# Kernel optimization log

Hardware: AMD Instinct MI355X
Metric: run time of the kernel (lower is better)

The kernel has to match this reference:

```python
import jax, jax.numpy as jnp
import numpy as np

HIDDEN = 2048
N_EXPERTS = 64
TOP_K = 2
N_TOKENS = 16384


def setup_inputs() -> dict:
    key = jax.random.key(0)
    k1, k2 = jax.random.split(key)
    x = jax.random.normal(k1, (N_TOKENS, HIDDEN), dtype=jnp.float32)
    gate_w = jax.random.normal(k2, (N_EXPERTS, HIDDEN), dtype=jnp.float32) * (1.0 / np.sqrt(HIDDEN))
    gate_b = jnp.zeros((N_EXPERTS,), dtype=jnp.float32)
    return {"x": x, "gate_w": gate_w, "gate_b": gate_b}


def reference(x, gate_w, gate_b):
    # gate: [N, H] @ [H, E] + [E] -> [N, E]
    router_logits = jnp.einsum("nh,eh->ne", x, gate_w) + gate_b
    # softmax over experts in fp32 (matches F.softmax(..., dim=1, dtype=float32))
    router_probs = jax.nn.softmax(router_logits.astype(jnp.float32), axis=1)
    # top-k experts per token
    router_weights, selected_experts_indices = jax.lax.top_k(router_probs, TOP_K)  # [N, K]
    router_weights = router_weights / jnp.sum(router_weights, axis=-1, keepdims=True)
    router_weights = router_weights.astype(x.dtype)
    # one-hot [N, K, E] -> permute(2,1,0) -> [E, K, N]
    expert_mask = jax.nn.one_hot(selected_experts_indices, N_EXPERTS, dtype=jnp.int64 if jax.config.jax_enable_x64 else jnp.int32)
    expert_mask = jnp.transpose(expert_mask, (2, 1, 0))
    return (router_logits, router_weights, selected_experts_indices, expert_mask)
```

## Files before the change

### kernel.cpp

```cpp
#include <hip/hip_runtime.h>
#include <hip/hip_bf16.h>
#include <math.h>

#define HIDDEN 2048
#define NEXP   64
#define NTOK   16384
#define NTGF   512

typedef __attribute__((ext_vector_type(8))) _Float16 f16x8;
typedef __attribute__((ext_vector_type(4))) float   f32x4;

__device__ __forceinline__ void split2_f16(float4 f0, float4 f1, f16x8& h, f16x8& l) {
    float e[8] = {f0.x, f0.y, f0.z, f0.w, f1.x, f1.y, f1.z, f1.w};
    f16x8 hv, lv;
#pragma unroll
    for (int i = 0; i < 8; ++i) {
        _Float16 hh = (_Float16)e[i];
        float r = e[i] - (float)hh;
        hv[i] = hh;
        lv[i] = (_Float16)r;
    }
    h = hv; l = lv;
}

__global__ __launch_bounds__(256) void prep_kernel(
    const float* __restrict__ gw, uint4* __restrict__ wh, uint4* __restrict__ wl)
{
    const int gid = blockIdx.x * 256 + threadIdx.x;
    const int c   = gid >> 9;
    const int e   = (gid >> 3) & 63;
    const int kgp = gid & 7;
    const int kg  = kgp ^ (e & 7);
    const float* src = gw + (size_t)e * HIDDEN + c * 64 + kg * 8;
    float4 s0 = *(const float4*)src;
    float4 s1 = *(const float4*)(src + 4);
    f16x8 h, l;
    split2_f16(s0, s1, h, l);
    wh[gid] = __builtin_bit_cast(uint4, h);
    wl[gid] = __builtin_bit_cast(uint4, l);
}

#define STAGE(cg, bo)                                                                     \
    _Pragma("unroll")                                                                     \
    for (int rr = 0; rr < 2; ++rr) {                                                      \
        const int s = rr * 256 + tid;                                                     \
        __builtin_amdgcn_global_load_lds(                                                 \
            (const __attribute__((address_space(1))) void*)(wh + (size_t)(cg) * 512 + s), \
            (__attribute__((address_space(3))) void*)&Bs[(bo) + s], 16, 0, 0);            \
        __builtin_amdgcn_global_load_lds(                                                 \
            (const __attribute__((address_space(1))) void*)(wl + (size_t)(cg) * 512 + s), \
            (__attribute__((address_space(3))) void*)&Bs[(bo) + 512 + s], 16, 0, 0);      \
    }

__global__ __launch_bounds__(256, 4) void gemm_kernel(
    const float* __restrict__ x,
    const uint4* __restrict__ wh,
    const uint4* __restrict__ wl,
    float* __restrict__ part,
    int klen)
{
    __shared__ uint4 Bs[2 * 1024];

    const int tid = threadIdx.x;
    const int l   = tid & 63;
    const int wv  = tid >> 6;
    const int kg  = blockIdx.y;
    const int kbase = kg * klen;
    const int nch   = klen >> 6;
    const int cg0   = kbase >> 6;
    const int t0    = blockIdx.x * 64 + wv * 16;

    const float4* xp = (const float4*)(x + (size_t)(t0 + (l & 15)) * HIDDEN + kbase) + ((l >> 4) * 2);

    const int lb = ((l & 15) << 3) | ((l >> 4) ^ (l & 7));

    f32x4 acc1[4], acc2[4];
#pragma unroll
    for (int eg = 0; eg < 4; ++eg) {
        acc1[eg] = (f32x4){0.f, 0.f, 0.f, 0.f};
        acc2[eg] = (f32x4){0.f, 0.f, 0.f, 0.f};
    }

    STAGE(cg0, 0)
    float4 a0 = xp[0], a1 = xp[1], a2 = xp[8], a3 = xp[9];
    __syncthreads();

    for (int c = 0; c < nch; ++c) {
        const int buf = c & 1;
        float4 n0 = a0, n1 = a1, n2 = a2, n3 = a3;
        if (c + 1 < nch) {
            STAGE(cg0 + c + 1, (buf ^ 1) * 1024)
            const int fb = (c + 1) * 16;
            n0 = xp[fb + 0]; n1 = xp[fb + 1]; n2 = xp[fb + 8]; n3 = xp[fb + 9];
        }

#pragma unroll
        for (int ks = 0; ks < 2; ++ks) {
            f16x8 ah, al;
            split2_f16(ks ? a2 : a0, ks ? a3 : a1, ah, al);
            const int ib = buf * 1024 + (lb ^ (ks << 2));
#pragma unroll
            for (int eg = 0; eg < 4; ++eg) {
                f16x8 bh = __builtin_bit_cast(f16x8, Bs[ib + eg * 128]);
                f16x8 bl = __builtin_bit_cast(f16x8, Bs[ib + 512 + eg * 128]);
                acc1[eg] = __builtin_amdgcn_mfma_f32_16x16x32_f16(ah, bh, acc1[eg], 0, 0, 0);
                acc2[eg] = __builtin_amdgcn_mfma_f32_16x16x32_f16(ah, bl, acc2[eg], 0, 0, 0);
                acc2[eg] = __builtin_amdgcn_mfma_f32_16x16x32_f16(al, bh, acc2[eg], 0, 0, 0);
            }
        }
        a0 = n0; a1 = n1; a2 = n2; a3 = n3;
        __syncthreads();
    }

    float* pp = part + ((size_t)kg * NTOK + t0) * NEXP;
#pragma unroll
    for (int eg = 0; eg < 4; ++eg)
#pragma unroll
        for (int i = 0; i < 4; ++i)
            pp[(size_t)((l >> 4) * 4 + i) * NEXP + eg * 16 + (l & 15)] =
                acc1[eg][i] + acc2[eg][i];
}

__global__ __launch_bounds__(256) void finish_kernel(
    const float* __restrict__ part,
    const float* __restrict__ bias_g,
    float* __restrict__ logits,
    float* __restrict__ weights,
    float* __restrict__ idxf,
    float* __restrict__ mask,
    int KS)
{
    __shared__ float Ls[32][65];
    __shared__ int selA[32], selB[32];

    const int tid = threadIdx.x;
    const int bm0 = blockIdx.x * 32;
    const int tn  = tid & 15;
    const int tm  = tid >> 4;

    float4 acc[2];
#pragma unroll
    for (int i = 0; i < 2; ++i) acc[i] = make_float4(0.f, 0.f, 0.f, 0.f);

    for (int kg = 0; kg < KS; ++kg) {
        const float* pb = part + ((size_t)kg * NTOK + bm0) * NEXP;
#pragma unroll
        for (int i = 0; i < 2; ++i) {
            float4 v = *(const float4*)&pb[(tm + 16 * i) * NEXP + 4 * tn];
            acc[i].x += v.x; acc[i].y += v.y; acc[i].z += v.z; acc[i].w += v.w;
        }
    }

    const float4 bv = *(const float4*)&bias_g[4 * tn];
#pragma unroll
    for (int i = 0; i < 2; ++i) {
        const int m = tm + 16 * i;
        float4 v;
        v.x = acc[i].x + bv.x;
        v.y = acc[i].y + bv.y;
        v.z = acc[i].z + bv.z;
        v.w = acc[i].w + bv.w;
        *(float4*)&logits[(size_t)(bm0 + m) * NEXP + 4 * tn] = v;
        Ls[m][4 * tn + 0] = v.x;
        Ls[m][4 * tn + 1] = v.y;
        Ls[m][4 * tn + 2] = v.z;
        Ls[m][4 * tn + 3] = v.w;
    }
    __syncthreads();

    if (tid < 32) {
        const int t = tid;
        float best = -1e30f, second = -1e30f;
        int bi = 0, si = 0;
#pragma unroll
        for (int e = 0; e < NEXP; ++e) {
            float v = Ls[t][e];
            if (v > best)        { second = best; si = bi; best = v; bi = e; }
            else if (v > second) { second = v; si = e; }
        }
        float r  = __expf(second - best);
        float w0 = 1.f / (1.f + r);
        float w1 = r / (1.f + r);
        const int tgl = bm0 + t;
        weights[2 * tgl + 0] = w0;
        weights[2 * tgl + 1] = w1;
        idxf[2 * tgl + 0] = (float)bi;
        idxf[2 * tgl + 1] = (float)si;
        selA[t] = bi;
        selB[t] = si;
    }
    __syncthreads();

    const int t8 = tid & 7;
    const int pg = tid >> 3;
    const int b0 = 4 * t8;
    int sA0 = selA[b0+0], sA1 = selA[b0+1], sA2 = selA[b0+2], sA3 = selA[b0+3];
    int sB0 = selB[b0+0], sB1 = selB[b0+1], sB2 = selB[b0+2], sB3 = selB[b0+3];
#pragma unroll
    for (int p = 0; p < 4; ++p) {
        const int pair = pg * 4 + p;
        const int e = pair >> 1;
        const int k = pair & 1;
        const int a0 = k ? sB0 : sA0, a1 = k ? sB1 : sA1, a2 = k ? sB2 : sA2, a3 = k ? sB3 : sA3;
        float4 v;
        v.x = (a0 == e) ? 1.f : 0.f;
        v.y = (a1 == e) ? 1.f : 0.f;
        v.z = (a2 == e) ? 1.f : 0.f;
        v.w = (a3 == e) ? 1.f : 0.f;
        *(float4*)&mask[((size_t)e * 2 + k) * NTOK + bm0 + b0] = v;
    }
}

extern "C" void kernel_launch(void* const* d_in, const int* in_sizes, int n_in,
                              void* d_out, int out_size, void* d_ws, size_t ws_size,
                              hipStream_t stream) {
    const float* x  = (const float*)d_in[0];
    const float* gw = (const float*)d_in[1];
    const float* gb = (const float*)d_in[2];

    float* out     = (float*)d_out;
    float* logits  = out;
    float* weights = out + (size_t)NTOK * NEXP;
    float* idxf    = weights + (size_t)NTOK * 2;
    float* mask    = idxf + (size_t)NTOK * 2;

    uint4* wh = (uint4*)d_ws;
    uint4* wl = wh + 16384;
    const size_t hdrB   = 2 * 16384 * sizeof(uint4);
    const size_t sliceB = (size_t)NTOK * NEXP * sizeof(float);
    int KS;
    float* part;
    if      (ws_size >= hdrB + 4 * sliceB) { KS = 4; part = (float*)((char*)d_ws + hdrB); }
    else if (ws_size >= hdrB + 2 * sliceB) { KS = 2; part = (float*)((char*)d_ws + hdrB); }
    else                                   { KS = 1; part = logits; }

    const int klen = HIDDEN / KS;
    prep_kernel<<<64, 256, 0, stream>>>(gw, wh, wl);
    dim3 gridA(NTOK / 64, KS);
    gemm_kernel<<<gridA, 256, 0, stream>>>(x, wh, wl, part, klen);
    finish_kernel<<<NTGF, 256, 0, stream>>>(part, gb, logits, weights, idxf, mask, KS);
}
```

Measured before the change: 45.57 us.

## Fuse GEMM and routing epilogue into one kernel and drop split-K

Combines the gate GEMM and the softmax/top-k/mask epilogue into a single kernel. Each block now covers the full hidden dimension for 64 tokens, adds the bias, and stages the logits in shared memory for top-2 selection and mask writes. This removes the split-K partial-sum buffer's global write and re-read, plus one kernel launch. In exchange the grid shrinks to 256 blocks of 4 waves each, which cuts memory-level parallelism while streaming x. It also drops the occupancy hint from the launch bounds.

```diff
diff --git a/kernel.cpp b/kernel.cpp
--- a/kernel.cpp
+++ b/kernel.cpp
@@ -5,7 +5,6 @@
 #define HIDDEN 2048
 #define NEXP   64
 #define NTOK   16384
-#define NTGF   512
 
 typedef __attribute__((ext_vector_type(8))) _Float16 f16x8;
 typedef __attribute__((ext_vector_type(4))) float   f32x4;
@@ -52,25 +51,27 @@
             (__attribute__((address_space(3))) void*)&Bs[(bo) + 512 + s], 16, 0, 0);      \
     }
 
-__global__ __launch_bounds__(256, 4) void gemm_kernel(
+__global__ __launch_bounds__(256) void fused_kernel(
     const float* __restrict__ x,
     const uint4* __restrict__ wh,
     const uint4* __restrict__ wl,
-    float* __restrict__ part,
-    int klen)
+    const float* __restrict__ bias_g,
+    float* __restrict__ logits,
+    float* __restrict__ weights,
+    float* __restrict__ idxf,
+    float* __restrict__ mask)
 {
     __shared__ uint4 Bs[2 * 1024];
+    __shared__ float Ls[64][65];
+    __shared__ int selA[64], selB[64];
 
     const int tid = threadIdx.x;
     const int l   = tid & 63;
     const int wv  = tid >> 6;
-    const int kg  = blockIdx.y;
-    const int kbase = kg * klen;
-    const int nch   = klen >> 6;
-    const int cg0   = kbase >> 6;
-    const int t0    = blockIdx.x * 64 + wv * 16;
+    const int tb0 = blockIdx.x * 64;
+    const int t0  = tb0 + wv * 16;
 
-    const float4* xp = (const float4*)(x + (size_t)(t0 + (l & 15)) * HIDDEN + kbase) + ((l >> 4) * 2);
+    const float4* xp = (const float4*)(x + (size_t)(t0 + (l & 15)) * HIDDEN) + ((l >> 4) * 2);
 
     const int lb = ((l & 15) << 3) | ((l >> 4) ^ (l & 7));
 
@@ -81,15 +82,16 @@
         acc2[eg] = (f32x4){0.f, 0.f, 0.f, 0.f};
     }
 
-    STAGE(cg0, 0)
+    STAGE(0, 0)
     float4 a0 = xp[0], a1 = xp[1], a2 = xp[8], a3 = xp[9];
     __syncthreads();
 
+    const int nch = HIDDEN / 64;
     for (int c = 0; c < nch; ++c) {
         const int buf = c & 1;
         float4 n0 = a0, n1 = a1, n2 = a2, n3 = a3;
         if (c + 1 < nch) {
-            STAGE(cg0 + c + 1, (buf ^ 1) * 1024)
+            STAGE(c + 1, (buf ^ 1) * 1024)
             const int fb = (c + 1) * 16;
             n0 = xp[fb + 0]; n1 = xp[fb + 1]; n2 = xp[fb + 8]; n3 = xp[fb + 9];
         }
@@ -112,63 +114,29 @@
         __syncthreads();
     }
 
-    float* pp = part + ((size_t)kg * NTOK + t0) * NEXP;
 #pragma unroll
-    for (int eg = 0; eg < 4; ++eg)
+    for (int eg = 0; eg < 4; ++eg) {
+        const float b = bias_g[eg * 16 + (l & 15)];
 #pragma unroll
         for (int i = 0; i < 4; ++i)
-            pp[(size_t)((l >> 4) * 4 + i) * NEXP + eg * 16 + (l & 15)] =
-                acc1[eg][i] + acc2[eg][i];
-}
-
-__global__ __launch_bounds__(256) void finish_kernel(
-    const float* __restrict__ part,
-    const float* __restrict__ bias_g,
-    float* __restrict__ logits,
-    float* __restrict__ weights,
-    float* __restrict__ idxf,
-    float* __restrict__ mask,
-    int KS)
-{
-    __shared__ float Ls[32][65];
-    __shared__ int selA[32], selB[32];
-
-    const int tid = threadIdx.x;
-    const int bm0 = blockIdx.x * 32;
-    const int tn  = tid & 15;
-    const int tm  = tid >> 4;
-
-    float4 acc[2];
-#pragma unroll
-    for (int i = 0; i < 2; ++i) acc[i] = make_float4(0.f, 0.f, 0.f, 0.f);
-
-    for (int kg = 0; kg < KS; ++kg) {
-        const float* pb = part + ((size_t)kg * NTOK + bm0) * NEXP;
-#pragma unroll
-        for (int i = 0; i < 2; ++i) {
-            float4 v = *(const float4*)&pb[(tm + 16 * i) * NEXP + 4 * tn];
-            acc[i].x += v.x; acc[i].y += v.y; acc[i].z += v.z; acc[i].w += v.w;
-        }
-    }
-
-    const float4 bv = *(const float4*)&bias_g[4 * tn];
-#pragma unroll
-    for (int i = 0; i < 2; ++i) {
-        const int m = tm + 16 * i;
-        float4 v;
-        v.x = acc[i].x + bv.x;
-        v.y = acc[i].y + bv.y;
-        v.z = acc[i].z + bv.z;
-        v.w = acc[i].w + bv.w;
-        *(float4*)&logits[(size_t)(bm0 + m) * NEXP + 4 * tn] = v;
-        Ls[m][4 * tn + 0] = v.x;
-        Ls[m][4 * tn + 1] = v.y;
-        Ls[m][4 * tn + 2] = v.z;
-        Ls[m][4 * tn + 3] = v.w;
+            Ls[wv * 16 + (l >> 4) * 4 + i][eg * 16 + (l & 15)] = acc1[eg][i] + acc2[eg][i] + b;
     }
     __syncthreads();
 
-    if (tid < 32) {
+#pragma unroll
+    for (int i = 0; i < 4; ++i) {
+        const int idx = i * 256 + tid;
+        const int row = idx >> 4;
+        const int c4  = (idx & 15) << 2;
+        float4 v;
+        v.x = Ls[row][c4 + 0];
+        v.y = Ls[row][c4 + 1];
+        v.z = Ls[row][c4 + 2];
+        v.w = Ls[row][c4 + 3];
+        *(float4*)&logits[(size_t)(tb0 + row) * NEXP + c4] = v;
+    }
+
+    if (tid < 64) {
         const int t = tid;
         float best = -1e30f, second = -1e30f;
         int bi = 0, si = 0;
@@ -181,7 +149,7 @@
         float r  = __expf(second - best);
         float w0 = 1.f / (1.f + r);
         float w1 = r / (1.f + r);
-        const int tgl = bm0 + t;
+        const int tgl = tb0 + t;
         weights[2 * tgl + 0] = w0;
         weights[2 * tgl + 1] = w1;
         idxf[2 * tgl + 0] = (float)bi;
@@ -191,14 +159,13 @@
     }
     __syncthreads();
 
-    const int t8 = tid & 7;
-    const int pg = tid >> 3;
-    const int b0 = 4 * t8;
-    int sA0 = selA[b0+0], sA1 = selA[b0+1], sA2 = selA[b0+2], sA3 = selA[b0+3];
-    int sB0 = selB[b0+0], sB1 = selB[b0+1], sB2 = selB[b0+2], sB3 = selB[b0+3];
+    const int t4 = tid & 15;
+    const int pg = tid >> 4;
+    int sA0 = selA[4*t4+0], sA1 = selA[4*t4+1], sA2 = selA[4*t4+2], sA3 = selA[4*t4+3];
+    int sB0 = selB[4*t4+0], sB1 = selB[4*t4+1], sB2 = selB[4*t4+2], sB3 = selB[4*t4+3];
 #pragma unroll
-    for (int p = 0; p < 4; ++p) {
-        const int pair = pg * 4 + p;
+    for (int p = 0; p < 8; ++p) {
+        const int pair = pg * 8 + p;
         const int e = pair >> 1;
         const int k = pair & 1;
         const int a0 = k ? sB0 : sA0, a1 = k ? sB1 : sA1, a2 = k ? sB2 : sA2, a3 = k ? sB3 : sA3;
@@ -207,7 +174,7 @@
         v.y = (a1 == e) ? 1.f : 0.f;
         v.z = (a2 == e) ? 1.f : 0.f;
         v.w = (a3 == e) ? 1.f : 0.f;
-        *(float4*)&mask[((size_t)e * 2 + k) * NTOK + bm0 + b0] = v;
+        *(float4*)&mask[((size_t)e * 2 + k) * NTOK + tb0 + 4 * t4] = v;
     }
 }
 
@@ -226,17 +193,7 @@
 
     uint4* wh = (uint4*)d_ws;
     uint4* wl = wh + 16384;
-    const size_t hdrB   = 2 * 16384 * sizeof(uint4);
-    const size_t sliceB = (size_t)NTOK * NEXP * sizeof(float);
-    int KS;
-    float* part;
-    if      (ws_size >= hdrB + 4 * sliceB) { KS = 4; part = (float*)((char*)d_ws + hdrB); }
-    else if (ws_size >= hdrB + 2 * sliceB) { KS = 2; part = (float*)((char*)d_ws + hdrB); }
-    else                                   { KS = 1; part = logits; }
 
-    const int klen = HIDDEN / KS;
     prep_kernel<<<64, 256, 0, stream>>>(gw, wh, wl);
-    dim3 gridA(NTOK / 64, KS);
-    gemm_kernel<<<gridA, 256, 0, stream>>>(x, wh, wl, part, klen);
-    finish_kernel<<<NTGF, 256, 0, stream>>>(part, gb, logits, weights, idxf, mask, KS);
+    fused_kernel<<<NTOK / 64, 256, 0, stream>>>(x, wh, wl, gb, logits, weights, idxf, mask);
 }
```

After: 58.69 us. 28.8% more time.

## Double per-wave token tile and K-chunk size to reuse staged weights

Applied to the files above, without the earlier changes.

Each wave now computes 32 tokens instead of 16, so every weight fragment read from LDS feeds two sets of MFMAs. Each stage also covers 128 K elements instead of 64, and the K loop is templated and fully unrolled. The block-level __syncthreads is replaced with a manual vmcnt wait plus s_barrier, so the prefetched x loads can stay in flight across the barrier. The cost is higher register pressure (launch bounds drop to 2 blocks per SM), doubled LDS use, and half as many blocks in the grid, which may reduce occupancy and latency hiding.

```diff
diff --git a/kernel.cpp b/kernel.cpp
--- a/kernel.cpp
+++ b/kernel.cpp
@@ -40,85 +40,113 @@
     wl[gid] = __builtin_bit_cast(uint4, l);
 }
 
-#define STAGE(cg, bo)                                                                     \
-    _Pragma("unroll")                                                                     \
-    for (int rr = 0; rr < 2; ++rr) {                                                      \
-        const int s = rr * 256 + tid;                                                     \
-        __builtin_amdgcn_global_load_lds(                                                 \
-            (const __attribute__((address_space(1))) void*)(wh + (size_t)(cg) * 512 + s), \
-            (__attribute__((address_space(3))) void*)&Bs[(bo) + s], 16, 0, 0);            \
-        __builtin_amdgcn_global_load_lds(                                                 \
-            (const __attribute__((address_space(1))) void*)(wl + (size_t)(cg) * 512 + s), \
-            (__attribute__((address_space(3))) void*)&Bs[(bo) + 512 + s], 16, 0, 0);      \
-    }
-
-__global__ __launch_bounds__(256, 4) void gemm_kernel(
+#define STAGE128(cc, bo)                                                                         \
+    _Pragma("unroll")                                                                            \
+    for (int rr = 0; rr < 4; ++rr) {                                                             \
+        const int s = rr * 256 + tid;                                                            \
+        __builtin_amdgcn_global_load_lds(                                                        \
+            (const __attribute__((address_space(1))) void*)(wh + (size_t)(cg0 + 2 * (cc)) * 512 + s), \
+            (__attribute__((address_space(3))) void*)&Bs[(bo) + s], 16, 0, 0);                   \
+        __builtin_amdgcn_global_load_lds(                                                        \
+            (const __attribute__((address_space(1))) void*)(wl + (size_t)(cg0 + 2 * (cc)) * 512 + s), \
+            (__attribute__((address_space(3))) void*)&Bs[(bo) + 1024 + s], 16, 0, 0);            \
+    }
+
+template<int NCH>
+__global__ __launch_bounds__(256, 2) void gemm_kernel(
     const float* __restrict__ x,
     const uint4* __restrict__ wh,
     const uint4* __restrict__ wl,
-    float* __restrict__ part,
-    int klen)
+    float* __restrict__ part)
 {
-    __shared__ uint4 Bs[2 * 1024];
+    __shared__ uint4 Bs[2 * 2048];
 
     const int tid = threadIdx.x;
     const int l   = tid & 63;
     const int wv  = tid >> 6;
     const int kg  = blockIdx.y;
-    const int kbase = kg * klen;
-    const int nch   = klen >> 6;
+    const int kbase = kg * (NCH * 128);
     const int cg0   = kbase >> 6;
-    const int t0    = blockIdx.x * 64 + wv * 16;
-
-    const float4* xp = (const float4*)(x + (size_t)(t0 + (l & 15)) * HIDDEN + kbase) + ((l >> 4) * 2);
+    const int t0    = blockIdx.x * 128 + wv * 32;
+
+    const float4* xp0 = (const float4*)(x + (size_t)(t0 + (l & 15)) * HIDDEN + kbase) + ((l >> 4) * 2);
+    const float4* xp1 = (const float4*)(x + (size_t)(t0 + 16 + (l & 15)) * HIDDEN + kbase) + ((l >> 4) * 2);
 
     const int lb = ((l & 15) << 3) | ((l >> 4) ^ (l & 7));
 
-    f32x4 acc1[4], acc2[4];
-#pragma unroll
-    for (int eg = 0; eg < 4; ++eg) {
-        acc1[eg] = (f32x4){0.f, 0.f, 0.f, 0.f};
-        acc2[eg] = (f32x4){0.f, 0.f, 0.f, 0.f};
-    }
-
-    STAGE(cg0, 0)
-    float4 a0 = xp[0], a1 = xp[1], a2 = xp[8], a3 = xp[9];
-    __syncthreads();
-
-    for (int c = 0; c < nch; ++c) {
+    f32x4 acc1[2][4], acc2[2][4];
+#pragma unroll
+    for (int r = 0; r < 2; ++r)
+#pragma unroll
+        for (int eg = 0; eg < 4; ++eg) {
+            acc1[r][eg] = (f32x4){0.f, 0.f, 0.f, 0.f};
+            acc2[r][eg] = (f32x4){0.f, 0.f, 0.f, 0.f};
+        }
+
+    float4 a[2][8], n[2][8];
+
+    STAGE128(0, 0)
+#pragma unroll
+    for (int j = 0; j < 4; ++j) {
+        a[0][2 * j] = xp0[j * 8]; a[0][2 * j + 1] = xp0[j * 8 + 1];
+        a[1][2 * j] = xp1[j * 8]; a[1][2 * j + 1] = xp1[j * 8 + 1];
+    }
+    asm volatile("s_waitcnt vmcnt(16)" ::: "memory");
+    __builtin_amdgcn_s_barrier();
+    __builtin_amdgcn_sched_barrier(0);
+
+#pragma unroll
+    for (int c = 0; c < NCH; ++c) {
         const int buf = c & 1;
-        float4 n0 = a0, n1 = a1, n2 = a2, n3 = a3;
-        if (c + 1 < nch) {
-            STAGE(cg0 + c + 1, (buf ^ 1) * 1024)
-            const int fb = (c + 1) * 16;
-            n0 = xp[fb + 0]; n1 = xp[fb + 1]; n2 = xp[fb + 8]; n3 = xp[fb + 9];
-        }
-
-#pragma unroll
-        for (int ks = 0; ks < 2; ++ks) {
-            f16x8 ah, al;
-            split2_f16(ks ? a2 : a0, ks ? a3 : a1, ah, al);
-            const int ib = buf * 1024 + (lb ^ (ks << 2));
+        if (c + 1 < NCH) {
+            STAGE128(c + 1, (buf ^ 1) * 2048)
+            const int fb = (c + 1) * 32;
+#pragma unroll
+            for (int j = 0; j < 4; ++j) {
+                n[0][2 * j] = xp0[fb + j * 8]; n[0][2 * j + 1] = xp0[fb + j * 8 + 1];
+                n[1][2 * j] = xp1[fb + j * 8]; n[1][2 * j + 1] = xp1[fb + j * 8 + 1];
+            }
+        }
+
+#pragma unroll
+        for (int ks = 0; ks < 4; ++ks) {
+            f16x8 ah0, al0, ah1, al1;
+            split2_f16(a[0][2 * ks], a[0][2 * ks + 1], ah0, al0);
+            split2_f16(a[1][2 * ks], a[1][2 * ks + 1], ah1, al1);
+            const int ib = buf * 2048 + (ks >> 1) * 512 + (lb ^ ((ks & 1) << 2));
 #pragma unroll
             for (int eg = 0; eg < 4; ++eg) {
                 f16x8 bh = __builtin_bit_cast(f16x8, Bs[ib + eg * 128]);
-                f16x8 bl = __builtin_bit_cast(f16x8, Bs[ib + 512 + eg * 128]);
-                acc1[eg] = __builtin_amdgcn_mfma_f32_16x16x32_f16(ah, bh, acc1[eg], 0, 0, 0);
-                acc2[eg] = __builtin_amdgcn_mfma_f32_16x16x32_f16(ah, bl, acc2[eg], 0, 0, 0);
-                acc2[eg] = __builtin_amdgcn_mfma_f32_16x16x32_f16(al, bh, acc2[eg], 0, 0, 0);
+                f16x8 bl = __builtin_bit_cast(f16x8, Bs[ib + 1024 + eg * 128]);
+                acc1[0][eg] = __builtin_amdgcn_mfma_f32_16x16x32_f16(ah0, bh, acc1[0][eg], 0, 0, 0);
+                acc2[0][eg] = __builtin_amdgcn_mfma_f32_16x16x32_f16(ah0, bl, acc2[0][eg], 0, 0, 0);
+                acc2[0][eg] = __builtin_amdgcn_mfma_f32_16x16x32_f16(al0, bh, acc2[0][eg], 0, 0, 0);
+                acc1[1][eg] = __builtin_amdgcn_mfma_f32_16x16x32_f16(ah1, bh, acc1[1][eg], 0, 0, 0);
+                acc2[1][eg] = __builtin_amdgcn_mfma_f32_16x16x32_f16(ah1, bl, acc2[1][eg], 0, 0, 0);
+                acc2[1][eg] = __builtin_amdgcn_mfma_f32_16x16x32_f16(al1, bh, acc2[1][eg], 0, 0, 0);
             }
         }
-        a0 = n0; a1 = n1; a2 = n2; a3 = n3;
-        __syncthreads();
+
+        if (c + 1 < NCH) {
+            asm volatile("s_waitcnt vmcnt(16)" ::: "memory");
+            __builtin_amdgcn_s_barrier();
+            __builtin_amdgcn_sched_barrier(0);
+#pragma unroll
+            for (int m = 0; m < 2; ++m)
+#pragma unroll
+                for (int j = 0; j < 8; ++j) a[m][j] = n[m][j];
+        }
     }
 
     float* pp = part + ((size_t)kg * NTOK + t0) * NEXP;
 #pragma unroll
-    for (int eg = 0; eg < 4; ++eg)
-#pragma unroll
-        for (int i = 0; i < 4; ++i)
-            pp[(size_t)((l >> 4) * 4 + i) * NEXP + eg * 16 + (l & 15)] =
-                acc1[eg][i] + acc2[eg][i];
+    for (int r = 0; r < 2; ++r)
+#pragma unroll
+        for (int eg = 0; eg < 4; ++eg)
+#pragma unroll
+            for (int i = 0; i < 4; ++i)
+                pp[(size_t)(r * 16 + (l >> 4) * 4 + i) * NEXP + eg * 16 + (l & 15)] =
+                    acc1[r][eg][i] + acc2[r][eg][i];
 }
 
 __global__ __launch_bounds__(256) void finish_kernel(
@@ -228,15 +256,15 @@
     uint4* wl = wh + 16384;
     const size_t hdrB   = 2 * 16384 * sizeof(uint4);
     const size_t sliceB = (size_t)NTOK * NEXP * sizeof(float);
-    int KS;
-    float* part;
-    if      (ws_size >= hdrB + 4 * sliceB) { KS = 4; part = (float*)((char*)d_ws + hdrB); }
-    else if (ws_size >= hdrB + 2 * sliceB) { KS = 2; part = (float*)((char*)d_ws + hdrB); }
-    else                                   { KS = 1; part = logits; }
-
-    const int klen = HIDDEN / KS;
+
     prep_kernel<<<64, 256, 0, stream>>>(gw, wh, wl);
-    dim3 gridA(NTOK / 64, KS);
-    gemm_kernel<<<gridA, 256, 0, stream>>>(x, wh, wl, part, klen);
-    finish_kernel<<<NTGF, 256, 0, stream>>>(part, gb, logits, weights, idxf, mask, KS);
-}
+
+    if (ws_size >= hdrB + 4 * sliceB) {
+        float* part = (float*)((char*)d_ws + hdrB);
+        gemm_kernel<4><<<dim3(NTOK / 128, 4), 256, 0, stream>>>(x, wh, wl, part);
+        finish_kernel<<<NTGF, 256, 0, stream>>>(part, gb, logits, weights, idxf, mask, 4);
+    } else {
+        gemm_kernel<16><<<dim3(NTOK / 128, 1), 256, 0, stream>>>(x, wh, wl, logits);
+        finish_kernel<<<NTGF, 256, 0, stream>>>(logits, gb, logits, weights, idxf, mask, 1);
+    }
+}
```

Result: slower. 51.70 us (+13.5%).
